# Performance work log

Measured on AMD Instinct MI355X. Metric: run time of the kernel, lower is better.

The kernel has to match this reference:

```python
import jax, jax.numpy as jnp
import numpy as np
import math

EMBED_DIM = 1024
NUM_HEADS = 16
HEAD_DIM = EMBED_DIM // NUM_HEADS
SCALING = HEAD_DIM ** -0.5
SOFTPLUS_BETA = math.log(2.0)


def linear(x, W, b):
    # torch nn.Linear: x @ W.T + b
    return jnp.einsum('...i,oi->...o', x, W) + b


def efficient_causal_attention_parallel(x, y, z):
    # x: (B, n, d1), y: (B, n, d1), z: (B, n, d2)
    n = x.shape[1]
    # outer products per step, then causal prefix-sum over n
    accum = jnp.cumsum(jnp.einsum('bni,bnj->bnij', y, z), axis=1)  # (B, n, d1, d2)
    res = jnp.einsum('bni,bnij->bnj', x, accum)                    # (B, n, d2)
    length_div = jnp.arange(1, n + 1, dtype=x.dtype)[None, :, None]
    return res / length_div


def setup_inputs() -> dict:
    key = jax.random.key(0)
    ks = jax.random.split(key, 12)
    tgt_len, bsz, plen = 2048, 2, 32
    E = EMBED_DIM
    s = 1.0 / math.sqrt(E)
    return {
        'query': jax.random.normal(ks[0], (tgt_len, bsz, E), jnp.float32),
        'pquery': jax.random.normal(ks[1], (plen, bsz, E), jnp.float32),
        'Wpq': jax.random.normal(ks[2], (E, E), jnp.float32) * s,
        'bpq': jnp.zeros((E,), jnp.float32),
        'Wq': jax.random.normal(ks[3], (E, E), jnp.float32) * s,
        'bq': jnp.zeros((E,), jnp.float32),
        'Wpc': jax.random.normal(ks[4], (E, E), jnp.float32) * s,
        'bpc': jnp.zeros((E,), jnp.float32),
        'Wc': jax.random.normal(ks[5], (E, E), jnp.float32) * s,
        'bc': jnp.zeros((E,), jnp.float32),
        'Wo': jax.random.normal(ks[6], (E, E), jnp.float32) * s,
        'bo': jnp.zeros((E,), jnp.float32),
    }


def reference(query, pquery, Wpq, bpq, Wq, bq, Wpc, bpc, Wc, bc, Wo, bo):
    tgt_len, bsz, E = query.shape
    plen = pquery.shape[0]
    H, D = NUM_HEADS, HEAD_DIM
    BH = bsz * H

    # pq: (plen, bsz, E) -> (bsz, H, plen, D), scaled
    pq = linear(pquery, Wpq, bpq).reshape(plen, bsz, H, D)
    pq = jnp.transpose(pq, (1, 2, 0, 3)) * SCALING

    # _compute_pattention: k (BH, tgt_len, D) @ pq^T (BH, D, plen)
    kp = linear(query, Wpc, bpc).reshape(tgt_len, BH, D).transpose(1, 0, 2)
    pqm = pq.reshape(BH, plen, D).transpose(0, 2, 1)  # (BH, D, plen)
    pattn = jnp.matmul(kp, pqm)                        # (BH, tgt_len, plen)
    pattn = jax.nn.softplus(SOFTPLUS_BETA * pattn) / SOFTPLUS_BETA

    q = (linear(query, Wq, bq) * SCALING).reshape(tgt_len, BH, D).transpose(1, 0, 2)
    kv = linear(query, Wc, bc).reshape(tgt_len, BH, D).transpose(1, 0, 2)  # tied k=v

    attn_weights = efficient_causal_attention_parallel(q, kv, pattn)  # (BH, tgt_len, plen)
    attn_weights = jax.nn.softmax(attn_weights, axis=-1)
    attn = efficient_causal_attention_parallel(attn_weights, pattn, kv)  # (BH, tgt_len, D)

    attn = attn.transpose(1, 0, 2).reshape(tgt_len, bsz, E)
    return linear(attn, Wo, bo)
```

## Files before the change

### kernel.cpp

```cpp
#include <hip/hip_runtime.h>
#include <hip/hip_bf16.h>
#include <math.h>

typedef __hip_bfloat16 bf16;
typedef __attribute__((ext_vector_type(8))) short bf16x8;
typedef __attribute__((ext_vector_type(4))) float f32x4;

__device__ __forceinline__ short f2bf_s(float v){ union{ bf16 b; short s;} u; u.b = __float2bfloat16(v); return u.s; }

__device__ __forceinline__ void gl_lds16(const bf16* g, short* l) {
    __builtin_amdgcn_global_load_lds(
        (const __attribute__((address_space(1))) void*)g,
        (__attribute__((address_space(3))) void*)l, 16, 0, 0);
}

#define LN2F 0.69314718055994531f

__device__ __forceinline__ void cvt_store4(bf16* d, size_t idx, float4 v) {
    union { ushort4 u; bf16 b[4]; } o;
    o.b[0] = __float2bfloat16(v.x);
    o.b[1] = __float2bfloat16(v.y);
    o.b[2] = __float2bfloat16(v.z);
    o.b[3] = __float2bfloat16(v.w);
    ((ushort4*)d)[idx] = o.u;
}

__device__ __forceinline__ void st_out(float* p, float v){ *p = v; }
__device__ __forceinline__ void st_out(bf16* p, float v){ *p = __float2bfloat16(v); }

__global__ __launch_bounds__(256)
void conv_all(const float* __restrict__ query, const float* __restrict__ pquery,
              const float* __restrict__ Wpq, const float* __restrict__ Wpc,
              const float* __restrict__ Wq, const float* __restrict__ Wc,
              const float* __restrict__ Wo,
              const float* __restrict__ bpc, const float* __restrict__ bq,
              const float* __restrict__ bc,
              bf16* __restrict__ qbf, bf16* __restrict__ pqy, bf16* __restrict__ wpq,
              bf16* __restrict__ wcat, bf16* __restrict__ wo_bf,
              float* __restrict__ biascat)
{
    int blk = blockIdx.x;
    if (blk < 4096) {
        int i = blk * 256 + threadIdx.x;
        cvt_store4(qbf, i, ((const float4*)query)[i]);
    } else if (blk < 4160) {
        int i = (blk - 4096) * 256 + threadIdx.x;
        cvt_store4(pqy, i, ((const float4*)pquery)[i]);
    } else if (blk < 5184) {
        int i = (blk - 4160) * 256 + threadIdx.x;
        cvt_store4(wpq, i, ((const float4*)Wpq)[i]);
    } else if (blk < 8256) {
        int rel = blk - 5184;
        const float* s = (rel < 1024) ? Wpc : ((rel < 2048) ? Wq : Wc);
        int i = (rel & 1023) * 256 + threadIdx.x;
        cvt_store4(wcat + (size_t)(rel >> 10) * 1048576, i, ((const float4*)s)[i]);
    } else if (blk < 9280) {
        int i = (blk - 8256) * 256 + threadIdx.x;
        cvt_store4(wo_bf, i, ((const float4*)Wo)[i]);
    } else {
        int i = (blk - 9280) * 256 + threadIdx.x;
        if (i < 3072) {
            float v = (i < 1024) ? bpc[i] : ((i < 2048) ? bq[i - 1024] : bc[i - 2048]);
            biascat[i] = v;
        }
    }
}

template<typename TO>
__global__ __launch_bounds__(256)
void gemm_bf16_nt(const bf16* __restrict__ A, const bf16* __restrict__ B,
                  const float* __restrict__ bias, TO* __restrict__ C,
                  int M, int N, int K, float scale_all, float scale_mid)
{
    __shared__ short As[128 * 32];
    __shared__ short Bs[128 * 32];

    const int tid  = threadIdx.x;
    const int lane = tid & 63;
    const int wave = tid >> 6;
    const int m0 = blockIdx.y * 128;
    const int n0 = blockIdx.x * 128;
    const int wm = (wave >> 1) * 64;
    const int wn = (wave & 1) * 64;

    f32x4 acc[4][4] = {};

    const int c0 = tid, c1 = tid + 256;
    const int r0 = c0 >> 2, s0 = c0 & 3;
    const int r1 = c1 >> 2, s1 = c1 & 3;

    const int kb = lane >> 4;
    const int rr = lane & 15;

    for (int k0 = 0; k0 < K; k0 += 32) {
        __syncthreads();
        gl_lds16(A + (size_t)(m0 + r0) * K + k0 + s0 * 8, As + c0 * 8);
        gl_lds16(A + (size_t)(m0 + r1) * K + k0 + s1 * 8, As + c1 * 8);
        gl_lds16(B + (size_t)(n0 + r0) * K + k0 + s0 * 8, Bs + c0 * 8);
        gl_lds16(B + (size_t)(n0 + r1) * K + k0 + s1 * 8, Bs + c1 * 8);
        __syncthreads();

        bf16x8 af[4], bfr[4];
        #pragma unroll
        for (int mi = 0; mi < 4; ++mi)
            af[mi] = *(const bf16x8*)(As + (wm + mi * 16 + rr) * 32 + kb * 8);
        #pragma unroll
        for (int ni = 0; ni < 4; ++ni)
            bfr[ni] = *(const bf16x8*)(Bs + (wn + ni * 16 + rr) * 32 + kb * 8);
        #pragma unroll
        for (int mi = 0; mi < 4; ++mi)
            #pragma unroll
            for (int ni = 0; ni < 4; ++ni)
                acc[mi][ni] = __builtin_amdgcn_mfma_f32_16x16x32_bf16(
                    af[mi], bfr[ni], acc[mi][ni], 0, 0, 0);
    }

    const int col_l = lane & 15;
    const int row_q = lane >> 4;
    #pragma unroll
    for (int ni = 0; ni < 4; ++ni) {
        int col = n0 + wn + ni * 16 + col_l;
        float bb = bias[col];
        float sc = ((col >> 10) == 1) ? scale_mid : scale_all;
        #pragma unroll
        for (int mi = 0; mi < 4; ++mi) {
            #pragma unroll
            for (int r = 0; r < 4; ++r) {
                int row = m0 + wm + mi * 16 + row_q * 4 + r;
                st_out(C + (size_t)row * N + col, sc * (acc[mi][ni][r] + bb));
            }
        }
    }
}

__global__ __launch_bounds__(256)
void gemm_bf16_nt64(const bf16* __restrict__ A, const bf16* __restrict__ B,
                    const float* __restrict__ bias, float* __restrict__ C,
                    int M, int N, int K)
{
    __shared__ short As[64 * 32];
    __shared__ short Bs[128 * 32];

    const int tid  = threadIdx.x;
    const int lane = tid & 63;
    const int wave = tid >> 6;
    const int m0 = blockIdx.y * 64;
    const int n0 = blockIdx.x * 128;
    const int wm = (wave >> 1) * 32;
    const int wn = (wave & 1) * 64;

    f32x4 acc[2][4] = {};

    const int ra = tid >> 2, sa = tid & 3;
    const int c0 = tid, c1 = tid + 256;
    const int rb0 = c0 >> 2, sb0 = c0 & 3;
    const int rb1 = c1 >> 2, sb1 = c1 & 3;

    const int kb = lane >> 4;
    const int rr = lane & 15;

    for (int k0 = 0; k0 < K; k0 += 32) {
        __syncthreads();
        gl_lds16(A + (size_t)(m0 + ra) * K + k0 + sa * 8, As + tid * 8);
        gl_lds16(B + (size_t)(n0 + rb0) * K + k0 + sb0 * 8, Bs + c0 * 8);
        gl_lds16(B + (size_t)(n0 + rb1) * K + k0 + sb1 * 8, Bs + c1 * 8);
        __syncthreads();

        bf16x8 af[2], bfr[4];
        #pragma unroll
        for (int mi = 0; mi < 2; ++mi)
            af[mi] = *(const bf16x8*)(As + (wm + mi * 16 + rr) * 32 + kb * 8);
        #pragma unroll
        for (int ni = 0; ni < 4; ++ni)
            bfr[ni] = *(const bf16x8*)(Bs + (wn + ni * 16 + rr) * 32 + kb * 8);
        #pragma unroll
        for (int mi = 0; mi < 2; ++mi)
            #pragma unroll
            for (int ni = 0; ni < 4; ++ni)
                acc[mi][ni] = __builtin_amdgcn_mfma_f32_16x16x32_bf16(
                    af[mi], bfr[ni], acc[mi][ni], 0, 0, 0);
    }

    const int col_l = lane & 15;
    const int row_q = lane >> 4;
    #pragma unroll
    for (int ni = 0; ni < 4; ++ni) {
        int col = n0 + wn + ni * 16 + col_l;
        float bb = bias[col];
        #pragma unroll
        for (int mi = 0; mi < 2; ++mi) {
            #pragma unroll
            for (int r = 0; r < 4; ++r) {
                int row = m0 + wm + mi * 16 + row_q * 4 + r;
                C[(size_t)row * N + col] = acc[mi][ni][r] + bb;
            }
        }
    }
}

__global__ __launch_bounds__(256)
void gemm_pq_partial(const bf16* __restrict__ A, const bf16* __restrict__ B,
                     float* __restrict__ part)
{
    __shared__ short As[64 * 32];
    __shared__ short Bs[128 * 32];

    const int tid  = threadIdx.x;
    const int lane = tid & 63;
    const int wave = tid >> 6;
    const int n0 = blockIdx.x * 128;
    const int kslice = blockIdx.y;
    const int kbase = kslice * 128;

    f32x4 acc[4][2] = {};

    const int ra = tid >> 2, sa = tid & 3;
    const int c0 = tid, c1 = tid + 256;
    const int rb0 = c0 >> 2, sb0 = c0 & 3;
    const int rb1 = c1 >> 2, sb1 = c1 & 3;

    const int kb = lane >> 4;
    const int rr = lane & 15;

    for (int k0 = kbase; k0 < kbase + 128; k0 += 32) {
        __syncthreads();
        gl_lds16(A + (size_t)ra * 1024 + k0 + sa * 8, As + tid * 8);
        gl_lds16(B + (size_t)(n0 + rb0) * 1024 + k0 + sb0 * 8, Bs + c0 * 8);
        gl_lds16(B + (size_t)(n0 + rb1) * 1024 + k0 + sb1 * 8, Bs + c1 * 8);
        __syncthreads();

        bf16x8 af[4], bfr[2];
        #pragma unroll
        for (int mi = 0; mi < 4; ++mi)
            af[mi] = *(const bf16x8*)(As + (mi * 16 + rr) * 32 + kb * 8);
        #pragma unroll
        for (int ni = 0; ni < 2; ++ni)
            bfr[ni] = *(const bf16x8*)(Bs + (wave * 32 + ni * 16 + rr) * 32 + kb * 8);
        #pragma unroll
        for (int mi = 0; mi < 4; ++mi)
            #pragma unroll
            for (int ni = 0; ni < 2; ++ni)
                acc[mi][ni] = __builtin_amdgcn_mfma_f32_16x16x32_bf16(
                    af[mi], bfr[ni], acc[mi][ni], 0, 0, 0);
    }

    const int col_l = lane & 15;
    const int row_q = lane >> 4;
    float* dst = part + (size_t)kslice * 65536;
    #pragma unroll
    for (int ni = 0; ni < 2; ++ni) {
        int col = n0 + wave * 32 + ni * 16 + col_l;
        #pragma unroll
        for (int mi = 0; mi < 4; ++mi) {
            #pragma unroll
            for (int r = 0; r < 4; ++r) {
                int row = mi * 16 + row_q * 4 + r;
                dst[(size_t)row * 1024 + col] = acc[mi][ni][r];
            }
        }
    }
}

__global__ __launch_bounds__(256)
void pq_reduce(const float* __restrict__ part, const float* __restrict__ bias,
               bf16* __restrict__ pq)
{
    int gid = blockIdx.x * 256 + threadIdx.x;
    int n = gid & 1023;
    float s = bias[n];
    #pragma unroll
    for (int k = 0; k < 8; ++k) s += part[(size_t)k * 65536 + gid];
    pq[gid] = __float2bfloat16(0.125f * s);
}

__global__ __launch_bounds__(256)
void pattn_sum_kernel(const bf16* __restrict__ kp, const bf16* __restrict__ kv,
                      const bf16* __restrict__ pqb, bf16* __restrict__ pattn,
                      float* __restrict__ Sbuf, int T, int ld)
{
    __shared__ short sKP[64 * 72];
    __shared__ short sKVT[64 * 72];
    __shared__ short sPQ[32 * 72];
    __shared__ short sPT[32 * 72];

    const int c = blockIdx.x, bh = blockIdx.y;
    const int b = bh >> 4, h = bh & 15;
    const int t0 = c * 64;
    const int tid = threadIdx.x;
    const int lane = tid & 63, wave = tid >> 6;
    const int rr = lane & 15, kb = lane >> 4;
    const int m0w = wave * 16;

    #pragma unroll
    for (int l = 0; l < 2; ++l) {
        int idx = tid + l * 256;
        int t = idx >> 3, d8 = (idx & 7) * 8;
        size_t g = (size_t)((t0 + t) * 2 + b) * ld + h * 64 + d8;
        uint4 vk = *(const uint4*)(kp + g);
        *(uint4*)(sKP + t * 72 + d8) = vk;
        uint4 vv = *(const uint4*)(kv + g + 2048);
        union { uint4 u; short s[8]; } cw; cw.u = vv;
        #pragma unroll
        for (int i = 0; i < 8; ++i) sKVT[(d8 + i) * 72 + t] = cw.s[i];
    }
    {
        int p = tid >> 3, d8 = (tid & 7) * 8;
        uint4 v = *(const uint4*)(pqb + (size_t)(p * 2 + b) * 1024 + h * 64 + d8);
        *(uint4*)(sPQ + p * 72 + d8) = v;
    }
    __syncthreads();

    {
        bf16x8 a0 = *(const bf16x8*)(sKP + (m0w + rr) * 72 + kb * 8);
        bf16x8 a1 = *(const bf16x8*)(sKP + (m0w + rr) * 72 + 32 + kb * 8);
        f32x4 acc[2] = {};
        #pragma unroll
        for (int nt = 0; nt < 2; ++nt) {
            bf16x8 b0 = *(const bf16x8*)(sPQ + (nt * 16 + rr) * 72 + kb * 8);
            bf16x8 b1 = *(const bf16x8*)(sPQ + (nt * 16 + rr) * 72 + 32 + kb * 8);
            acc[nt] = __builtin_amdgcn_mfma_f32_16x16x32_bf16(a0, b0, acc[nt], 0, 0, 0);
            acc[nt] = __builtin_amdgcn_mfma_f32_16x16x32_bf16(a1, b1, acc[nt], 0, 0, 0);
        }
        #pragma unroll
        for (int nt = 0; nt < 2; ++nt)
            #pragma unroll
            for (int r = 0; r < 4; ++r) {
                int t = m0w + kb * 4 + r;
                int p = nt * 16 + rr;
                float z = LN2F * acc[nt][r];
                float sp = (fmaxf(z, 0.f) + log1pf(__expf(-fabsf(z)))) / LN2F;
                short sb = f2bf_s(sp);
                sPT[p * 72 + t] = sb;
                ((unsigned short*)pattn)[((size_t)bh * T + t0 + t) * 32 + p] = (unsigned short)sb;
            }
    }
    __syncthreads();

    {
        bf16x8 a0 = *(const bf16x8*)(sKVT + (m0w + rr) * 72 + kb * 8);
        bf16x8 a1 = *(const bf16x8*)(sKVT + (m0w + rr) * 72 + 32 + kb * 8);
        f32x4 acc[2] = {};
        #pragma unroll
        for (int nt = 0; nt < 2; ++nt) {
            bf16x8 b0 = *(const bf16x8*)(sPT + (nt * 16 + rr) * 72 + kb * 8);
            bf16x8 b1 = *(const bf16x8*)(sPT + (nt * 16 + rr) * 72 + 32 + kb * 8);
            acc[nt] = __builtin_amdgcn_mfma_f32_16x16x32_bf16(a0, b0, acc[nt], 0, 0, 0);
            acc[nt] = __builtin_amdgcn_mfma_f32_16x16x32_bf16(a1, b1, acc[nt], 0, 0, 0);
        }
        float* Sdst = Sbuf + ((size_t)bh * 32 + c) * 2048;
        #pragma unroll
        for (int nt = 0; nt < 2; ++nt)
            #pragma unroll
            for (int r = 0; r < 4; ++r) {
                int i = m0w + kb * 4 + r;
                int j = nt * 16 + rr;
                Sdst[i * 32 + j] = acc[nt][r];
            }
    }
}

__global__ __launch_bounds__(256)
void prefix_state_kernel(float* __restrict__ Sbuf)
{
    const int NCH = 32;
    int gid = blockIdx.x * 256 + threadIdx.x;
    int bh = gid >> 11, e = gid & 2047;
    float* p = Sbuf + (size_t)bh * NCH * 2048 + e;
    float run = 0.f;
    #pragma unroll
    for (int c = 0; c < NCH; ++c) {
        float t = p[c * 2048];
        p[c * 2048] = run;
        run += t;
    }
}

__global__ __launch_bounds__(256)
void chunk_attn(const bf16* __restrict__ qg, const bf16* __restrict__ kvg,
                const bf16* __restrict__ pg, const float* __restrict__ Sg,
                bf16* __restrict__ attn, int T, int ld)
{
    __shared__ short sm[26112];
    short* sQ   = sm;
    short* sKV  = sm + 4608;
    short* sW   = sm + 9216;
    short* sAW  = sm + 13824;
    short* sS   = sm + 16384;
    short* sST  = sm + 18944;
    short* sP   = sm + 21248;
    short* sPT  = sm + 23808;

    const int bh = blockIdx.y, c = blockIdx.x;
    const int b = bh >> 4, h = bh & 15;
    const int t0 = c * 64;
    const int tid = threadIdx.x;
    const int lane = tid & 63;
    const int wave = tid >> 6;
    const int rr = lane & 15;
    const int kb = lane >> 4;
    const int m0w = wave * 16;
    const float* Sblk = Sg + ((size_t)bh * 32 + c) * 2048;

    #pragma unroll
    for (int l = 0; l < 2; ++l) {
        int idx = tid + l * 256;
        int t = idx >> 3, d8 = (idx & 7) * 8;
        size_t g = (size_t)((t0 + t) * 2 + b) * ld + h * 64 + d8;
        uint4 qv = *(const uint4*)(qg + g);
        *(uint4*)(sQ + t * 72 + d8) = qv;
        uint4 kvv = *(const uint4*)(kvg + g);
        *(uint4*)(sKV + t * 72 + d8) = kvv;
    }
    {
        int t = tid >> 2, j8 = (tid & 3) * 8;
        uint4 pv = *(const uint4*)(pg + ((size_t)bh * T + t0 + t) * 32 + j8);
        *(uint4*)(sP + t * 40 + j8) = pv;
        union { uint4 u; short s[8]; } cp; cp.u = pv;
        #pragma unroll
        for (int i = 0; i < 8; ++i) sPT[(j8 + i) * 72 + t] = cp.s[i];

        float4 s0 = *(const float4*)(Sblk + t * 32 + j8);
        float4 s1 = *(const float4*)(Sblk + t * 32 + j8 + 4);
        union { ushort4 u; short s[4]; bf16 bb[4]; } c0, c1;
        c0.bb[0] = __float2bfloat16(s0.x);
        c0.bb[1] = __float2bfloat16(s0.y);
        c0.bb[2] = __float2bfloat16(s0.z);
        c0.bb[3] = __float2bfloat16(s0.w);
        c1.bb[0] = __float2bfloat16(s1.x);
        c1.bb[1] = __float2bfloat16(s1.y);
        c1.bb[2] = __float2bfloat16(s1.z);
        c1.bb[3] = __float2bfloat16(s1.w);
        *(ushort4*)(sS + t * 40 + j8) = c0.u;
        *(ushort4*)(sS + t * 40 + j8 + 4) = c1.u;
        #pragma unroll
        for (int i = 0; i < 4; ++i) sST[(j8 + i) * 72 + t] = c0.s[i];
        #pragma unroll
        for (int i = 0; i < 4; ++i) sST[(j8 + 4 + i) * 72 + t] = c1.s[i];
    }
    __syncthreads();

    {
        bf16x8 aq0 = *(const bf16x8*)(sQ + (m0w + rr) * 72 + kb * 8);
        bf16x8 aq1 = *(const bf16x8*)(sQ + (m0w + rr) * 72 + 32 + kb * 8);
        f32x4 acc[4] = {};
        #pragma unroll
        for (int nt = 0; nt < 4; ++nt) {
            bf16x8 b0 = *(const bf16x8*)(sKV + (nt * 16 + rr) * 72 + kb * 8);
            bf16x8 b1 = *(const bf16x8*)(sKV + (nt * 16 + rr) * 72 + 32 + kb * 8);
            acc[nt] = __builtin_amdgcn_mfma_f32_16x16x32_bf16(aq0, b0, acc[nt], 0, 0, 0);
            acc[nt] = __builtin_amdgcn_mfma_f32_16x16x32_bf16(aq1, b1, acc[nt], 0, 0, 0);
        }
        #pragma unroll
        for (int nt = 0; nt < 4; ++nt)
            #pragma unroll
            for (int r = 0; r < 4; ++r) {
                int t = m0w + kb * 4 + r;
                int s = nt * 16 + rr;
                sW[t * 72 + s] = f2bf_s((s <= t) ? acc[nt][r] : 0.f);
            }
    }
    __syncthreads();

    {
        bf16x8 aq0 = *(const bf16x8*)(sQ + (m0w + rr) * 72 + kb * 8);
        bf16x8 aq1 = *(const bf16x8*)(sQ + (m0w + rr) * 72 + 32 + kb * 8);
        bf16x8 aw0 = *(const bf16x8*)(sW + (m0w + rr) * 72 + kb * 8);
        bf16x8 aw1 = *(const bf16x8*)(sW + (m0w + rr) * 72 + 32 + kb * 8);
        f32x4 acc[2] = {};
        #pragma unroll
        for (int nt = 0; nt < 2; ++nt) {
            bf16x8 bs0 = *(const bf16x8*)(sST + (nt * 16 + rr) * 72 + kb * 8);
            bf16x8 bs1 = *(const bf16x8*)(sST + (nt * 16 + rr) * 72 + 32 + kb * 8);
            bf16x8 bp0 = *(const bf16x8*)(sPT + (nt * 16 + rr) * 72 + kb * 8);
            bf16x8 bp1 = *(const bf16x8*)(sPT + (nt * 16 + rr) * 72 + 32 + kb * 8);
            acc[nt] = __builtin_amdgcn_mfma_f32_16x16x32_bf16(aq0, bs0, acc[nt], 0, 0, 0);
            acc[nt] = __builtin_amdgcn_mfma_f32_16x16x32_bf16(aq1, bs1, acc[nt], 0, 0, 0);
            acc[nt] = __builtin_amdgcn_mfma_f32_16x16x32_bf16(aw0, bp0, acc[nt], 0, 0, 0);
            acc[nt] = __builtin_amdgcn_mfma_f32_16x16x32_bf16(aw1, bp1, acc[nt], 0, 0, 0);
        }
        #pragma unroll
        for (int r = 0; r < 4; ++r) {
            int t = m0w + kb * 4 + r;
            float inv_len = 1.0f / (float)(t0 + t + 1);
            float v0 = acc[0][r] * inv_len;
            float v1 = acc[1][r] * inv_len;
            float m = fmaxf(v0, v1);
            m = fmaxf(m, __shfl_xor(m, 1));
            m = fmaxf(m, __shfl_xor(m, 2));
            m = fmaxf(m, __shfl_xor(m, 4));
            m = fmaxf(m, __shfl_xor(m, 8));
            float e0 = __expf(v0 - m), e1 = __expf(v1 - m);
            float s = e0 + e1;
            s += __shfl_xor(s, 1);
            s += __shfl_xor(s, 2);
            s += __shfl_xor(s, 4);
            s += __shfl_xor(s, 8);
            float rs = 1.0f / s;
            sAW[t * 40 + rr]      = f2bf_s(e0 * rs);
            sAW[t * 40 + 16 + rr] = f2bf_s(e1 * rs);
        }
    }
    __syncthreads();

    short* sKVT = sQ;
    {
        #pragma unroll
        for (int l = 0; l < 2; ++l) {
            int idx = tid + l * 256;
            int t = idx >> 3, d8 = (idx & 7) * 8;
            union { uint4 u; short s[8]; } ck;
            ck.u = *(const uint4*)(sKV + t * 72 + d8);
            #pragma unroll
            for (int i = 0; i < 8; ++i) sKVT[(d8 + i) * 72 + t] = ck.s[i];
        }
        bf16x8 aa = *(const bf16x8*)(sAW + (m0w + rr) * 40 + kb * 8);
        f32x4 acc[4] = {};
        #pragma unroll
        for (int nt = 0; nt < 4; ++nt) {
            bf16x8 bp = *(const bf16x8*)(sP + (nt * 16 + rr) * 40 + kb * 8);
            acc[nt] = __builtin_amdgcn_mfma_f32_16x16x32_bf16(aa, bp, acc[nt], 0, 0, 0);
        }
        __syncthreads();
        #pragma unroll
        for (int nt = 0; nt < 4; ++nt)
            #pragma unroll
            for (int r = 0; r < 4; ++r) {
                int t = m0w + kb * 4 + r;
                int s = nt * 16 + rr;
                sW[t * 72 + s] = f2bf_s((s <= t) ? acc[nt][r] : 0.f);
            }
    }
    __syncthreads();

    {
        bf16x8 aa  = *(const bf16x8*)(sAW + (m0w + rr) * 40 + kb * 8);
        bf16x8 ap0 = *(const bf16x8*)(sW + (m0w + rr) * 72 + kb * 8);
        bf16x8 ap1 = *(const bf16x8*)(sW + (m0w + rr) * 72 + 32 + kb * 8);
        f32x4 acc[4] = {};
        #pragma unroll
        for (int nt = 0; nt < 4; ++nt) {
            bf16x8 bs = *(const bf16x8*)(sS + (nt * 16 + rr) * 40 + kb * 8);
            bf16x8 bk0 = *(const bf16x8*)(sKVT + (nt * 16 + rr) * 72 + kb * 8);
            bf16x8 bk1 = *(const bf16x8*)(sKVT + (nt * 16 + rr) * 72 + 32 + kb * 8);
            acc[nt] = __builtin_amdgcn_mfma_f32_16x16x32_bf16(aa,  bs,  acc[nt], 0, 0, 0);
            acc[nt] = __builtin_amdgcn_mfma_f32_16x16x32_bf16(ap0, bk0, acc[nt], 0, 0, 0);
            acc[nt] = __builtin_amdgcn_mfma_f32_16x16x32_bf16(ap1, bk1, acc[nt], 0, 0, 0);
        }
        #pragma unroll
        for (int nt = 0; nt < 4; ++nt)
            #pragma unroll
            for (int r = 0; r < 4; ++r) {
                int t = m0w + kb * 4 + r;
                int d = nt * 16 + rr;
                float v = acc[nt][r] / (float)(t0 + t + 1);
                ((unsigned short*)attn)[((size_t)((t0 + t) * 2 + b)) * 1024 + h * 64 + d] =
                    (unsigned short)f2bf_s(v);
            }
    }
}

extern "C" void kernel_launch(void* const* d_in, const int* in_sizes, int n_in,
                              void* d_out, int out_size, void* d_ws, size_t ws_size,
                              hipStream_t stream) {
    const float* query  = (const float*)d_in[0];
    const float* pquery = (const float*)d_in[1];
    const float* Wpq = (const float*)d_in[2];
    const float* bpq = (const float*)d_in[3];
    const float* Wq  = (const float*)d_in[4];
    const float* bq  = (const float*)d_in[5];
    const float* Wpc = (const float*)d_in[6];
    const float* bpc = (const float*)d_in[7];
    const float* Wc  = (const float*)d_in[8];
    const float* bc  = (const float*)d_in[9];
    const float* Wo  = (const float*)d_in[10];
    const float* bo  = (const float*)d_in[11];
    float* out = (float*)d_out;

    const int T = 2048, E = 1024, MROWS = 4096;
    const int NCH = 32;

    float* ws = (float*)d_ws;
    float* pq_f      = ws;
    float* Cbig_f    = pq_f + 65536;
    float* pattn_f   = Cbig_f + 6291456;
    float* S_buf     = pattn_f + 1048576;
    float* qbf_f     = S_buf + 2097152;
    float* wcat_f    = qbf_f + 2097152;
    float* wo_f      = wcat_f + 1572864;
    float* wpq_f     = wo_f + 524288;

    bf16* pq_bf   = (bf16*)pq_f;
    bf16* Cbig    = (bf16*)Cbig_f;
    bf16* pattn_bf= (bf16*)pattn_f;
    bf16* qbf     = (bf16*)qbf_f;
    bf16* wcat    = (bf16*)wcat_f;
    bf16* wo_bf   = (bf16*)wo_f;
    bf16* wpq_bf  = (bf16*)wpq_f;
    bf16* pqy_bf  = (bf16*)pattn_f;
    float* biascat = pattn_f + 32768;
    float* pq_part = S_buf;
    bf16* attn_bf = qbf;

    conv_all<<<9292, 256, 0, stream>>>(query, pquery, Wpq, Wpc, Wq, Wc, Wo,
                                       bpc, bq, bc, qbf, pqy_bf, wpq_bf,
                                       wcat, wo_bf, biascat);
    gemm_pq_partial<<<dim3(8, 8), 256, 0, stream>>>(pqy_bf, wpq_bf, pq_part);
    pq_reduce<<<256, 256, 0, stream>>>(pq_part, bpq, pq_bf);

    gemm_bf16_nt<bf16><<<dim3(24, 32), 256, 0, stream>>>(
        qbf, wcat, biascat, Cbig, MROWS, 3072, E, 1.0f, 0.125f);

    pattn_sum_kernel<<<dim3(NCH, 32), 256, 0, stream>>>(
        Cbig, Cbig, pq_bf, pattn_bf, S_buf, T, 3072);
    prefix_state_kernel<<<256, 256, 0, stream>>>(S_buf);
    chunk_attn<<<dim3(NCH, 32), 256, 0, stream>>>(
        Cbig + 1024, Cbig + 2048, pattn_bf, S_buf, attn_bf, T, 3072);
    gemm_bf16_nt64<<<dim3(8, 64), 256, 0, stream>>>(
        attn_bf, wo_bf, bo, out, MROWS, E, E);
}
```

Before: 190.9 us.

## Fuse pq projection GEMM into main QKV GEMM launch and deepen K tile to 64

Merges the small pquery projection partial GEMM into the large fused QKV GEMM as extra blocks in the same grid, removing one kernel launch and letting the small work overlap with the big GEMM. Both the fused GEMM and the output-projection GEMM now load a 64-wide K step per iteration as two 32-wide slabs, halving the number of barrier pairs per K loop. This doubles LDS use per block, which may lower occupancy. Extra grid blocks beyond the 64 pq tiles exit immediately.

```diff
diff --git a/kernel.cpp b/kernel.cpp
--- a/kernel.cpp
+++ b/kernel.cpp
@@ -24,9 +24,6 @@
     o.b[3] = __float2bfloat16(v.w);
     ((ushort4*)d)[idx] = o.u;
 }
-
-__device__ __forceinline__ void st_out(float* p, float v){ *p = v; }
-__device__ __forceinline__ void st_out(bf16* p, float v){ *p = __float2bfloat16(v); }
 
 __global__ __launch_bounds__(256)
 void conv_all(const float* __restrict__ query, const float* __restrict__ pquery,
@@ -66,68 +63,126 @@
     }
 }
 
-template<typename TO>
 __global__ __launch_bounds__(256)
-void gemm_bf16_nt(const bf16* __restrict__ A, const bf16* __restrict__ B,
-                  const float* __restrict__ bias, TO* __restrict__ C,
-                  int M, int N, int K, float scale_all, float scale_mid)
+void gemm_fused(const bf16* __restrict__ A, const bf16* __restrict__ B,
+                const float* __restrict__ bias, bf16* __restrict__ C,
+                int M, int N, int K, float scale_all, float scale_mid,
+                const bf16* __restrict__ pqA, const bf16* __restrict__ pqB,
+                float* __restrict__ part)
 {
-    __shared__ short As[128 * 32];
-    __shared__ short Bs[128 * 32];
+    __shared__ short As[8192];
+    __shared__ short Bs[8192];
 
     const int tid  = threadIdx.x;
     const int lane = tid & 63;
     const int wave = tid >> 6;
-    const int m0 = blockIdx.y * 128;
-    const int n0 = blockIdx.x * 128;
-    const int wm = (wave >> 1) * 64;
-    const int wn = (wave & 1) * 64;
-
-    f32x4 acc[4][4] = {};
-
-    const int c0 = tid, c1 = tid + 256;
-    const int r0 = c0 >> 2, s0 = c0 & 3;
-    const int r1 = c1 >> 2, s1 = c1 & 3;
-
     const int kb = lane >> 4;
     const int rr = lane & 15;
 
-    for (int k0 = 0; k0 < K; k0 += 32) {
-        __syncthreads();
-        gl_lds16(A + (size_t)(m0 + r0) * K + k0 + s0 * 8, As + c0 * 8);
-        gl_lds16(A + (size_t)(m0 + r1) * K + k0 + s1 * 8, As + c1 * 8);
-        gl_lds16(B + (size_t)(n0 + r0) * K + k0 + s0 * 8, Bs + c0 * 8);
-        gl_lds16(B + (size_t)(n0 + r1) * K + k0 + s1 * 8, Bs + c1 * 8);
-        __syncthreads();
-
-        bf16x8 af[4], bfr[4];
-        #pragma unroll
-        for (int mi = 0; mi < 4; ++mi)
-            af[mi] = *(const bf16x8*)(As + (wm + mi * 16 + rr) * 32 + kb * 8);
-        #pragma unroll
-        for (int ni = 0; ni < 4; ++ni)
-            bfr[ni] = *(const bf16x8*)(Bs + (wn + ni * 16 + rr) * 32 + kb * 8);
-        #pragma unroll
-        for (int mi = 0; mi < 4; ++mi)
-            #pragma unroll
-            for (int ni = 0; ni < 4; ++ni)
-                acc[mi][ni] = __builtin_amdgcn_mfma_f32_16x16x32_bf16(
-                    af[mi], bfr[ni], acc[mi][ni], 0, 0, 0);
-    }
-
-    const int col_l = lane & 15;
-    const int row_q = lane >> 4;
-    #pragma unroll
-    for (int ni = 0; ni < 4; ++ni) {
-        int col = n0 + wn + ni * 16 + col_l;
-        float bb = bias[col];
-        float sc = ((col >> 10) == 1) ? scale_mid : scale_all;
-        #pragma unroll
-        for (int mi = 0; mi < 4; ++mi) {
-            #pragma unroll
-            for (int r = 0; r < 4; ++r) {
-                int row = m0 + wm + mi * 16 + row_q * 4 + r;
-                st_out(C + (size_t)row * N + col, sc * (acc[mi][ni][r] + bb));
+    if (blockIdx.y < 32) {
+        const int m0 = blockIdx.y * 128;
+        const int n0 = blockIdx.x * 128;
+        const int wm = (wave >> 1) * 64;
+        const int wn = (wave & 1) * 64;
+
+        f32x4 acc[4][4] = {};
+
+        for (int k0 = 0; k0 < K; k0 += 64) {
+            __syncthreads();
+            #pragma unroll
+            for (int l = 0; l < 4; ++l) {
+                int cc = tid + l * 256;
+                int row = (cc >> 2) & 127;
+                int slab = cc >> 9;
+                int ks8 = cc & 3;
+                gl_lds16(A + (size_t)(m0 + row) * K + k0 + slab * 32 + ks8 * 8, As + cc * 8);
+                gl_lds16(B + (size_t)(n0 + row) * K + k0 + slab * 32 + ks8 * 8, Bs + cc * 8);
+            }
+            __syncthreads();
+
+            #pragma unroll
+            for (int ks = 0; ks < 2; ++ks) {
+                bf16x8 af[4], bfr[4];
+                #pragma unroll
+                for (int mi = 0; mi < 4; ++mi)
+                    af[mi] = *(const bf16x8*)(As + ks * 4096 + (wm + mi * 16 + rr) * 32 + kb * 8);
+                #pragma unroll
+                for (int ni = 0; ni < 4; ++ni)
+                    bfr[ni] = *(const bf16x8*)(Bs + ks * 4096 + (wn + ni * 16 + rr) * 32 + kb * 8);
+                #pragma unroll
+                for (int mi = 0; mi < 4; ++mi)
+                    #pragma unroll
+                    for (int ni = 0; ni < 4; ++ni)
+                        acc[mi][ni] = __builtin_amdgcn_mfma_f32_16x16x32_bf16(
+                            af[mi], bfr[ni], acc[mi][ni], 0, 0, 0);
+            }
+        }
+
+        const int col_l = lane & 15;
+        const int row_q = lane >> 4;
+        #pragma unroll
+        for (int ni = 0; ni < 4; ++ni) {
+            int col = n0 + wn + ni * 16 + col_l;
+            float bb = bias[col];
+            float sc = ((col >> 10) == 1) ? scale_mid : scale_all;
+            #pragma unroll
+            for (int mi = 0; mi < 4; ++mi) {
+                #pragma unroll
+                for (int r = 0; r < 4; ++r) {
+                    int row = m0 + wm + mi * 16 + row_q * 4 + r;
+                    C[(size_t)row * N + col] = __float2bfloat16(sc * (acc[mi][ni][r] + bb));
+                }
+            }
+        }
+    } else {
+        int pqIdx = (blockIdx.y - 32) * 24 + blockIdx.x;
+        if (pqIdx >= 64) return;
+        const int n0 = (pqIdx & 7) * 128;
+        const int kslice = pqIdx >> 3;
+        const int kbase = kslice * 128;
+
+        f32x4 acc[4][2] = {};
+
+        const int ra = tid >> 2, sa = tid & 3;
+        const int c0 = tid, c1 = tid + 256;
+        const int rb0 = c0 >> 2, sb0 = c0 & 3;
+        const int rb1 = c1 >> 2, sb1 = c1 & 3;
+
+        for (int k0 = kbase; k0 < kbase + 128; k0 += 32) {
+            __syncthreads();
+            gl_lds16(pqA + (size_t)ra * 1024 + k0 + sa * 8, As + tid * 8);
+            gl_lds16(pqB + (size_t)(n0 + rb0) * 1024 + k0 + sb0 * 8, Bs + c0 * 8);
+            gl_lds16(pqB + (size_t)(n0 + rb1) * 1024 + k0 + sb1 * 8, Bs + c1 * 8);
+            __syncthreads();
+
+            bf16x8 af[4], bfr[2];
+            #pragma unroll
+            for (int mi = 0; mi < 4; ++mi)
+                af[mi] = *(const bf16x8*)(As + (mi * 16 + rr) * 32 + kb * 8);
+            #pragma unroll
+            for (int ni = 0; ni < 2; ++ni)
+                bfr[ni] = *(const bf16x8*)(Bs + (wave * 32 + ni * 16 + rr) * 32 + kb * 8);
+            #pragma unroll
+            for (int mi = 0; mi < 4; ++mi)
+                #pragma unroll
+                for (int ni = 0; ni < 2; ++ni)
+                    acc[mi][ni] = __builtin_amdgcn_mfma_f32_16x16x32_bf16(
+                        af[mi], bfr[ni], acc[mi][ni], 0, 0, 0);
+        }
+
+        const int col_l = lane & 15;
+        const int row_q = lane >> 4;
+        float* dst = part + (size_t)kslice * 65536;
+        #pragma unroll
+        for (int ni = 0; ni < 2; ++ni) {
+            int col = n0 + wave * 32 + ni * 16 + col_l;
+            #pragma unroll
+            for (int mi = 0; mi < 4; ++mi) {
+                #pragma unroll
+                for (int r = 0; r < 4; ++r) {
+                    int row = mi * 16 + row_q * 4 + r;
+                    dst[(size_t)row * 1024 + col] = acc[mi][ni][r];
+                }
             }
         }
     }
@@ -138,8 +193,8 @@
                     const float* __restrict__ bias, float* __restrict__ C,
                     int M, int N, int K)
 {
-    __shared__ short As[64 * 32];
-    __shared__ short Bs[128 * 32];
+    __shared__ short As[4096];
+    __shared__ short Bs[8192];
 
     const int tid  = threadIdx.x;
     const int lane = tid & 63;
@@ -151,34 +206,45 @@
 
     f32x4 acc[2][4] = {};
 
-    const int ra = tid >> 2, sa = tid & 3;
-    const int c0 = tid, c1 = tid + 256;
-    const int rb0 = c0 >> 2, sb0 = c0 & 3;
-    const int rb1 = c1 >> 2, sb1 = c1 & 3;
-
     const int kb = lane >> 4;
     const int rr = lane & 15;
 
-    for (int k0 = 0; k0 < K; k0 += 32) {
+    for (int k0 = 0; k0 < K; k0 += 64) {
         __syncthreads();
-        gl_lds16(A + (size_t)(m0 + ra) * K + k0 + sa * 8, As + tid * 8);
-        gl_lds16(B + (size_t)(n0 + rb0) * K + k0 + sb0 * 8, Bs + c0 * 8);
-        gl_lds16(B + (size_t)(n0 + rb1) * K + k0 + sb1 * 8, Bs + c1 * 8);
+        #pragma unroll
+        for (int l = 0; l < 2; ++l) {
+            int cc = tid + l * 256;
+            int row = (cc >> 2) & 63;
+            int slab = cc >> 8;
+            int ks8 = cc & 3;
+            gl_lds16(A + (size_t)(m0 + row) * K + k0 + slab * 32 + ks8 * 8, As + cc * 8);
+        }
+        #pragma unroll
+        for (int l = 0; l < 4; ++l) {
+            int cc = tid + l * 256;
+            int row = (cc >> 2) & 127;
+            int slab = cc >> 9;
+            int ks8 = cc & 3;
+            gl_lds16(B + (size_t)(n0 + row) * K + k0 + slab * 32 + ks8 * 8, Bs + cc * 8);
+        }
         __syncthreads();
 
-        bf16x8 af[2], bfr[4];
-        #pragma unroll
-        for (int mi = 0; mi < 2; ++mi)
-            af[mi] = *(const bf16x8*)(As + (wm + mi * 16 + rr) * 32 + kb * 8);
-        #pragma unroll
-        for (int ni = 0; ni < 4; ++ni)
-            bfr[ni] = *(const bf16x8*)(Bs + (wn + ni * 16 + rr) * 32 + kb * 8);
-        #pragma unroll
-        for (int mi = 0; mi < 2; ++mi)
+        #pragma unroll
+        for (int ks = 0; ks < 2; ++ks) {
+            bf16x8 af[2], bfr[4];
+            #pragma unroll
+            for (int mi = 0; mi < 2; ++mi)
+                af[mi] = *(const bf16x8*)(As + ks * 2048 + (wm + mi * 16 + rr) * 32 + kb * 8);
             #pragma unroll
             for (int ni = 0; ni < 4; ++ni)
-                acc[mi][ni] = __builtin_amdgcn_mfma_f32_16x16x32_bf16(
-                    af[mi], bfr[ni], acc[mi][ni], 0, 0, 0);
+                bfr[ni] = *(const bf16x8*)(Bs + ks * 4096 + (wn + ni * 16 + rr) * 32 + kb * 8);
+            #pragma unroll
+            for (int mi = 0; mi < 2; ++mi)
+                #pragma unroll
+                for (int ni = 0; ni < 4; ++ni)
+                    acc[mi][ni] = __builtin_amdgcn_mfma_f32_16x16x32_bf16(
+                        af[mi], bfr[ni], acc[mi][ni], 0, 0, 0);
+        }
     }
 
     const int col_l = lane & 15;
@@ -193,69 +259,6 @@
             for (int r = 0; r < 4; ++r) {
                 int row = m0 + wm + mi * 16 + row_q * 4 + r;
                 C[(size_t)row * N + col] = acc[mi][ni][r] + bb;
-            }
-        }
-    }
-}
-
-__global__ __launch_bounds__(256)
-void gemm_pq_partial(const bf16* __restrict__ A, const bf16* __restrict__ B,
-                     float* __restrict__ part)
-{
-    __shared__ short As[64 * 32];
-    __shared__ short Bs[128 * 32];
-
-    const int tid  = threadIdx.x;
-    const int lane = tid & 63;
-    const int wave = tid >> 6;
-    const int n0 = blockIdx.x * 128;
-    const int kslice = blockIdx.y;
-    const int kbase = kslice * 128;
-
-    f32x4 acc[4][2] = {};
-
-    const int ra = tid >> 2, sa = tid & 3;
-    const int c0 = tid, c1 = tid + 256;
-    const int rb0 = c0 >> 2, sb0 = c0 & 3;
-    const int rb1 = c1 >> 2, sb1 = c1 & 3;
-
-    const int kb = lane >> 4;
-    const int rr = lane & 15;
-
-    for (int k0 = kbase; k0 < kbase + 128; k0 += 32) {
-        __syncthreads();
-        gl_lds16(A + (size_t)ra * 1024 + k0 + sa * 8, As + tid * 8);
-        gl_lds16(B + (size_t)(n0 + rb0) * 1024 + k0 + sb0 * 8, Bs + c0 * 8);
-        gl_lds16(B + (size_t)(n0 + rb1) * 1024 + k0 + sb1 * 8, Bs + c1 * 8);
-        __syncthreads();
-
-        bf16x8 af[4], bfr[2];
-        #pragma unroll
-        for (int mi = 0; mi < 4; ++mi)
-            af[mi] = *(const bf16x8*)(As + (mi * 16 + rr) * 32 + kb * 8);
-        #pragma unroll
-        for (int ni = 0; ni < 2; ++ni)
-            bfr[ni] = *(const bf16x8*)(Bs + (wave * 32 + ni * 16 + rr) * 32 + kb * 8);
-        #pragma unroll
-        for (int mi = 0; mi < 4; ++mi)
-            #pragma unroll
-            for (int ni = 0; ni < 2; ++ni)
-                acc[mi][ni] = __builtin_amdgcn_mfma_f32_16x16x32_bf16(
-                    af[mi], bfr[ni], acc[mi][ni], 0, 0, 0);
-    }
-
-    const int col_l = lane & 15;
-    const int row_q = lane >> 4;
-    float* dst = part + (size_t)kslice * 65536;
-    #pragma unroll
-    for (int ni = 0; ni < 2; ++ni) {
-        int col = n0 + wave * 32 + ni * 16 + col_l;
-        #pragma unroll
-        for (int mi = 0; mi < 4; ++mi) {
-            #pragma unroll
-            for (int r = 0; r < 4; ++r) {
-                int row = mi * 16 + row_q * 4 + r;
-                dst[(size_t)row * 1024 + col] = acc[mi][ni][r];
             }
         }
     }
@@ -604,12 +607,10 @@
     conv_all<<<9292, 256, 0, stream>>>(query, pquery, Wpq, Wpc, Wq, Wc, Wo,
                                        bpc, bq, bc, qbf, pqy_bf, wpq_bf,
                                        wcat, wo_bf, biascat);
-    gemm_pq_partial<<<dim3(8, 8), 256, 0, stream>>>(pqy_bf, wpq_bf, pq_part);
+    gemm_fused<<<dim3(24, 35), 256, 0, stream>>>(
+        qbf, wcat, biascat, Cbig, MROWS, 3072, E, 1.0f, 0.125f,
+        pqy_bf, wpq_bf, pq_part);
     pq_reduce<<<256, 256, 0, stream>>>(pq_part, bpq, pq_bf);
-
-    gemm_bf16_nt<bf16><<<dim3(24, 32), 256, 0, stream>>>(
-        qbf, wcat, biascat, Cbig, MROWS, 3072, E, 1.0f, 0.125f);
-
     pattn_sum_kernel<<<dim3(NCH, 32), 256, 0, stream>>>(
         Cbig, Cbig, pq_bf, pattn_bf, S_buf, T, 3072);
     prefix_state_kernel<<<256, 256, 0, stream>>>(S_buf);
```

After: 193.8 us. About the same (+1.5%).
